# Kernel optimization log

Measured on AMD Instinct MI355X. Metric: run time of the kernel, lower is better.

## Reference

```python
import jax, jax.numpy as jnp
import numpy as np

K = 9  # neighbors per node (Dynamic_GraphConv2d k, dilation=1)


def setup_inputs() -> dict:
    key = jax.random.key(0)
    k1, k2 = jax.random.split(key, 2)
    x = jax.random.normal(k1, (2, 128, 64, 64), dtype=jnp.float32)
    # EdgeConv2d nn: 1x1 conv mapping 2*in_channels -> out_channels
    w = jax.random.normal(k2, (256, 256), dtype=jnp.float32) * 0.05  # [out, 2*in]
    b = jnp.zeros((256,), dtype=jnp.float32)
    return {"x": x, "w": w, "b": b}


def _knn_graph(xf, k):
    # xf: [B, C, N]. DenseDilatedKnnGraph L2-normalizes features before kNN.
    xn = xf * jax.lax.rsqrt(jnp.sum(xf * xf, axis=1, keepdims=True) + 1e-12)
    xt = jnp.transpose(xn, (0, 2, 1))                  # [B, N, C]
    sq = jnp.sum(xt * xt, axis=-1)                     # [B, N]
    inner = jnp.einsum('bnc,bmc->bnm', xt, xt)         # [B, N, N]
    neg_dist = 2.0 * inner - sq[:, :, None] - sq[:, None, :]
    _, nn_idx = jax.lax.top_k(neg_dist, k)             # [B, N, k] nearest neighbors
    return nn_idx


def reference(x, w, b):
    B, C, H, W = x.shape
    N = H * W
    xf = x.reshape(B, C, N)                            # nodes = flattened spatial dims
    nn_idx = _knn_graph(xf, K)
    # gather neighbor features x_j: [B, C, N, k]
    xt = jnp.transpose(xf, (0, 2, 1))                  # [B, N, C]
    x_j = jax.vmap(lambda t, i: t[i])(xt, nn_idx)      # [B, N, k, C]
    x_j = jnp.transpose(x_j, (0, 3, 1, 2))             # [B, C, N, k]
    x_i = xf[:, :, :, None]                            # center features [B, C, N, 1]
    # EdgeConv: max_k relu(W @ concat(x_i, x_j - x_i) + b)
    feat = jnp.concatenate(
        [jnp.broadcast_to(x_i, x_j.shape), x_j - x_i], axis=1)  # [B, 2C, N, k]
    out = jnp.einsum('oc,bcnk->bonk', w, feat) + b[None, :, None, None]
    out = jax.nn.relu(out)
    out = jnp.max(out, axis=-1)                        # [B, O, N]
    return out.reshape(B, -1, H, W)
```

## Files before the change

### kernel.cpp

```cpp
#include <hip/hip_runtime.h>
#include <float.h>

constexpr int CB = 2;
constexpr int CC = 128;
constexpr int CN = 4096;
constexpr int NSPLIT = 16;

typedef unsigned long long u64;
typedef unsigned int u32;

constexpr size_t OFF_SQ = 0;
constexpr size_t OFF_WT = OFF_SQ + (size_t)CB * CN;
constexpr size_t OFF_A  = OFF_WT + (size_t)CC * 512;
constexpr size_t OFF_PK = OFF_A + (size_t)CB * CN * 256;
constexpr size_t OFF_NN = OFF_PK + (size_t)CB * CN * NSPLIT * 12 / 1;

typedef __attribute__((ext_vector_type(8))) short bf16x8;
typedef __attribute__((ext_vector_type(4))) float f32x4;

__device__ __forceinline__ unsigned short f2bf(float f) {
    u32 u = __float_as_uint(f);
    u32 r = (u + 0x7FFFu + ((u >> 16) & 1u)) >> 16;
    return (unsigned short)r;
}
__device__ __forceinline__ float bf2f(unsigned short h) {
    return __uint_as_float(((u32)h) << 16);
}

__device__ __forceinline__ u32 mono32(float v) {
    u32 u = __float_as_uint(v);
    u32 m = (u32)((int)u >> 31);
    return u ^ (m | 0x80000000u);
}
__device__ __forceinline__ u64 make_key(float v, int jg) {
    return ((u64)mono32(v) << 12) | (u32)(4095 - jg);
}
__device__ __forceinline__ void key_insert(u64 (&sk)[9], u64 key) {
    u64 t = key;
#pragma unroll
    for (int k = 0; k < 9; ++k) {
        const bool gt = t > sk[k];
        const u64 hi = gt ? t : sk[k];
        t = gt ? sk[k] : t;
        sk[k] = hi;
    }
}
__device__ __forceinline__ void key_init(u64 (&sk)[9]) {
#pragma unroll
    for (int k = 0; k < 9; ++k) sk[k] = (u64)(8 - k);
}

__global__ __launch_bounds__(256) void prep_kernel(const float* __restrict__ x,
                                                   float* __restrict__ sqv,
                                                   unsigned short* __restrict__ xh,
                                                   unsigned short* __restrict__ xm,
                                                   unsigned short* __restrict__ xl) {
    __shared__ float XT[128][65];
    __shared__ float red[4][64];
    __shared__ float invl[64];
    const int b = blockIdx.y, n0 = blockIdx.x * 64;
    const int tid = threadIdx.x;
    const int nl = tid & 63, c0 = tid >> 6;
#pragma unroll 4
    for (int cc = 0; cc < 32; ++cc) {
        int c = cc * 4 + c0;
        XT[c][nl] = x[((size_t)(b * 128 + c)) * 4096 + n0 + nl];
    }
    __syncthreads();
    {
        float acc = 0.f;
#pragma unroll 4
        for (int cc = 0; cc < 32; ++cc) { float v = XT[c0 * 32 + cc][nl]; acc += v * v; }
        red[c0][nl] = acc;
    }
    __syncthreads();
    if (tid < 64) {
        float ss = red[0][tid] + red[1][tid] + red[2][tid] + red[3][tid] + 1e-12f;
        invl[tid] = 1.0f / sqrtf(ss);
    }
    __syncthreads();
    {
        float acc = 0.f;
        float iv = invl[nl];
#pragma unroll 4
        for (int cc = 0; cc < 32; ++cc) {
            int c = cc * 4 + c0;
            float v = XT[c][nl] * iv;
            XT[c][nl] = v;
            acc += v * v;
        }
        red[c0][nl] = acc;
    }
    __syncthreads();
    if (tid < 64) {
        sqv[b * 4096 + n0 + tid] = red[0][tid] + red[1][tid] + red[2][tid] + red[3][tid];
    }
    __syncthreads();
    {
        const int n = tid & 63, cq = tid >> 6;
        unsigned short hs[32], ms[32], ls[32];
#pragma unroll
        for (int cc = 0; cc < 32; ++cc) {
            float v = XT[cq * 32 + cc][n];
            unsigned short h = f2bf(v);  float hf = bf2f(h);
            float r1 = v - hf;
            unsigned short m = f2bf(r1); float mf = bf2f(m);
            unsigned short l = f2bf(r1 - mf);
            hs[cc] = h; ms[cc] = m; ls[cc] = l;
        }
        const int g = (n0 >> 4) + (n >> 4), r = n & 15;
        const size_t gb = ((size_t)(b * 256 + g)) * 2048 + r * 8;
#pragma unroll
        for (int u = 0; u < 4; ++u) {
            const size_t off = gb + (size_t)(cq * 4 + u) * 128;
            *(float4*)&xh[off] = *(const float4*)&hs[u * 8];
            *(float4*)&xm[off] = *(const float4*)&ms[u * 8];
            *(float4*)&xl[off] = *(const float4*)&ls[u * 8];
        }
    }
}

__global__ __launch_bounds__(256) void wprep_kernel(const float* __restrict__ w,
                                                    float* __restrict__ wt) {
    int id = blockIdx.x * 256 + threadIdx.x;
    int c = id >> 9, o = id & 511;
    float v;
    if (o < 256) v = w[o * 256 + c] - w[o * 256 + 128 + c];
    else         v = w[(o - 256) * 256 + 128 + c];
    wt[c * 512 + o] = v;
}

__global__ __launch_bounds__(256, 4) void knn_kernel(const unsigned short* __restrict__ xh,
                                                     const unsigned short* __restrict__ xm,
                                                     const unsigned short* __restrict__ xl,
                                                     const float* __restrict__ sqv,
                                                     u32* __restrict__ pk) {
    __shared__ u64 MK[2304];

    const int b  = blockIdx.z;
    const int i0 = blockIdx.y * 64;
    const int js = blockIdx.x;
    const int tid = threadIdx.x;
    const int lane = tid & 63, w = tid >> 6;
    const int l15 = lane & 15, l4 = lane >> 4;

    const size_t ib0 = ((size_t)(b * 256 + (i0 >> 4) + w)) * 2048;
    u64 sk[9];
    key_init(sk);

    for (int tt = 0; tt < 4; ++tt) {
        const int t = (tt + w) & 3;
        const int jt = js * 256 + t * 64;
        const size_t jb0 = ((size_t)(b * 256 + (jt >> 4))) * 2048;
        f32x4 a0 = {0.f, 0.f, 0.f, 0.f}, a1 = a0, a2 = a0, a3 = a0;

#pragma unroll
        for (int ch = 0; ch < 4; ++ch) {
            const int koff = (ch * 4 + l4) * 128 + l15 * 8;
            const bf16x8 ih = *(const bf16x8*)(xh + ib0 + koff);
            const bf16x8 im = *(const bf16x8*)(xm + ib0 + koff);
            const bf16x8 il = *(const bf16x8*)(xl + ib0 + koff);
#define DO_Y(ACC, Y)                                                          \
            {                                                                 \
                const bf16x8 jh = *(const bf16x8*)(xh + jb0 + (Y) * 2048 + koff); \
                const bf16x8 jm = *(const bf16x8*)(xm + jb0 + (Y) * 2048 + koff); \
                const bf16x8 jl = *(const bf16x8*)(xl + jb0 + (Y) * 2048 + koff); \
                ACC = __builtin_amdgcn_mfma_f32_16x16x32_bf16(jh, ih, ACC, 0, 0, 0); \
                ACC = __builtin_amdgcn_mfma_f32_16x16x32_bf16(jh, im, ACC, 0, 0, 0); \
                ACC = __builtin_amdgcn_mfma_f32_16x16x32_bf16(jm, ih, ACC, 0, 0, 0); \
                ACC = __builtin_amdgcn_mfma_f32_16x16x32_bf16(jm, im, ACC, 0, 0, 0); \
                ACC = __builtin_amdgcn_mfma_f32_16x16x32_bf16(jh, il, ACC, 0, 0, 0); \
                ACC = __builtin_amdgcn_mfma_f32_16x16x32_bf16(jl, ih, ACC, 0, 0, 0); \
            }
            DO_Y(a0, 0) DO_Y(a1, 1) DO_Y(a2, 2) DO_Y(a3, 3)
#undef DO_Y
        }
#define SCAN_Y(ACC, Y)                                                        \
        {                                                                     \
            const int jb4 = jt + (Y) * 16 + l4 * 4;                           \
            const float4 sq4 = *(const float4*)&sqv[b * 4096 + jb4];          \
            key_insert(sk, make_key(fmaf(2.0f, ACC[0], -sq4.x), jb4 + 0));    \
            key_insert(sk, make_key(fmaf(2.0f, ACC[1], -sq4.y), jb4 + 1));    \
            key_insert(sk, make_key(fmaf(2.0f, ACC[2], -sq4.z), jb4 + 2));    \
            key_insert(sk, make_key(fmaf(2.0f, ACC[3], -sq4.w), jb4 + 3));    \
        }
        SCAN_Y(a0, 0) SCAN_Y(a1, 1) SCAN_Y(a2, 2) SCAN_Y(a3, 3)
#undef SCAN_Y
    }
#pragma unroll
    for (int k = 0; k < 9; ++k) MK[tid * 9 + k] = sk[k];
    __syncthreads();
    if (tid < 64) {
        u64 mk[9];
        key_init(mk);
        const int wsrc = tid >> 4, r = tid & 15;
        for (int q2 = 0; q2 < 4; ++q2) {
            const int src = wsrc * 64 + q2 * 16 + r;
            for (int k = 0; k < 9; ++k) key_insert(mk, MK[src * 9 + k]);
        }
        u32 ow[12];
        u32 iw0 = 0, iw1 = 0, iw2 = 0;
#pragma unroll
        for (int k = 0; k < 9; ++k) {
            ow[k] = (u32)(mk[k] >> 12);
            u32 lj = (u32)((4095 - (int)(mk[k] & 4095)) - js * 256) & 255u;
            if (k < 4)      iw0 |= lj << (k * 8);
            else if (k < 8) iw1 |= lj << ((k - 4) * 8);
            else            iw2 |= lj;
        }
        ow[9] = iw0; ow[10] = iw1; ow[11] = iw2;
        const size_t base = ((size_t)(b * 4096 + i0 + tid) * NSPLIT + js) * 12;
        *(uint4*)&pk[base]     = *(const uint4*)&ow[0];
        *(uint4*)&pk[base + 4] = *(const uint4*)&ow[4];
        *(uint4*)&pk[base + 8] = *(const uint4*)&ow[8];
    }
}

__global__ __launch_bounds__(64) void merge_kernel(const u32* __restrict__ pk,
                                                   int* __restrict__ nn) {
    int t = blockIdx.x * 64 + threadIdx.x;
    u64 mk[9];
    key_init(mk);
    for (int s = 0; s < NSPLIT; ++s) {
        const u32* p = pk + ((size_t)t * NSPLIT + s) * 12;
        u32 ow[12];
        *(uint4*)&ow[0] = *(const uint4*)&p[0];
        *(uint4*)&ow[4] = *(const uint4*)&p[4];
        *(uint4*)&ow[8] = *(const uint4*)&p[8];
        const u32 iw[3] = {ow[9], ow[10], ow[11]};
#pragma unroll
        for (int k = 0; k < 9; ++k) {
            const int lj = (int)((iw[k >> 2] >> ((k & 3) * 8)) & 255u);
            const int jg = s * 256 + lj;
            const u64 key = ((u64)ow[k] << 12) | (u32)(4095 - jg);
            key_insert(mk, key);
        }
    }
#pragma unroll
    for (int k = 0; k < 9; ++k) nn[t * 9 + k] = 4095 - (int)(mk[k] & 4095);
}

__global__ __launch_bounds__(256, 2) void pq_kernel(const float* __restrict__ x,
                                                    const float* __restrict__ wt,
                                                    float* __restrict__ q,
                                                    float* __restrict__ out) {
    __shared__ float Xs[128][64];
    __shared__ float Ws[128][64];
    const int b = blockIdx.z;
    const int n0 = blockIdx.x * 64;
    const int o0 = blockIdx.y * 64;
    const int tid = threadIdx.x;
    {
        const int c4 = tid >> 4, j4 = (tid & 15) * 4;
#pragma unroll
        for (int cc = 0; cc < 8; ++cc) {
            int c = cc * 16 + c4;
            *(float4*)&Xs[c][j4] = *(const float4*)&x[((size_t)(b * 128 + c)) * 4096 + n0 + j4];
            *(float4*)&Ws[c][j4] = *(const float4*)&wt[c * 512 + o0 + j4];
        }
    }
    __syncthreads();
    const int tx = tid & 15, ty = tid >> 4;
    float acc[4][4];
#pragma unroll
    for (int i = 0; i < 4; ++i)
#pragma unroll
        for (int j = 0; j < 4; ++j) acc[i][j] = 0.f;
#pragma unroll 4
    for (int c = 0; c < 128; ++c) {
        const float4 av = *(const float4*)&Xs[c][ty * 4];
        const float4 bv = *(const float4*)&Ws[c][tx * 4];
        const float ar[4] = {av.x, av.y, av.z, av.w};
        const float br[4] = {bv.x, bv.y, bv.z, bv.w};
#pragma unroll
        for (int i = 0; i < 4; ++i)
#pragma unroll
            for (int j = 0; j < 4; ++j) acc[i][j] = fmaf(ar[i], br[j], acc[i][j]);
    }
    if (o0 < 256) {
#pragma unroll
        for (int j = 0; j < 4; ++j) {
            float4 v = make_float4(acc[0][j], acc[1][j], acc[2][j], acc[3][j]);
            *(float4*)&out[((size_t)(b * 256 + o0 + tx * 4 + j)) * 4096 + n0 + ty * 4] = v;
        }
    } else {
#pragma unroll
        for (int i = 0; i < 4; ++i) {
            float4 v = make_float4(acc[i][0], acc[i][1], acc[i][2], acc[i][3]);
            *(float4*)&q[((size_t)(b * 4096 + n0 + ty * 4 + i)) * 256 + (o0 - 256) + tx * 4] = v;
        }
    }
}

__global__ __launch_bounds__(256) void gather_kernel(const float* __restrict__ q,
                                                     const int* __restrict__ nn,
                                                     const float* __restrict__ bias,
                                                     float* __restrict__ out) {
    __shared__ int idx[32][9];
    const int b = blockIdx.y, n0 = blockIdx.x * 32;
    const int tid = threadIdx.x;
    for (int t = tid; t < 288; t += 256) {
        int pt = t / 9, k = t - pt * 9;
        idx[pt][k] = nn[(b * 4096 + n0 + pt) * 9 + k];
    }
    __syncthreads();
    const float bv = bias[tid];
    const size_t orow = ((size_t)(b * 256 + tid)) * 4096 + n0;
    float pvals[32];
#pragma unroll
    for (int u = 0; u < 8; ++u)
        *(float4*)&pvals[u * 4] = *(const float4*)&out[orow + u * 4];
    float val[32];
#pragma unroll
    for (int pt = 0; pt < 32; ++pt) {
        float m = -FLT_MAX;
#pragma unroll
        for (int k = 0; k < 9; ++k) {
            int j = idx[pt][k] & 4095;
            m = fmaxf(m, q[((size_t)(b * 4096 + j)) * 256 + tid]);
        }
        float vv = pvals[pt] + bv + m;
        val[pt] = vv > 0.f ? vv : 0.f;
    }
#pragma unroll
    for (int u = 0; u < 8; ++u) {
        float4 v = make_float4(val[u * 4], val[u * 4 + 1], val[u * 4 + 2], val[u * 4 + 3]);
        *(float4*)&out[orow + u * 4] = v;
    }
}

extern "C" void kernel_launch(void* const* d_in, const int* in_sizes, int n_in,
                              void* d_out, int out_size, void* d_ws, size_t ws_size,
                              hipStream_t stream) {
    const float* x    = (const float*)d_in[0];
    const float* w    = (const float*)d_in[1];
    const float* bias = (const float*)d_in[2];
    float* ws = (float*)d_ws;
    float* sq = ws + OFF_SQ;
    float* wt = ws + OFF_WT;
    unsigned short* xh = (unsigned short*)(ws + OFF_A);
    unsigned short* xm = xh + (size_t)CB * CN * CC;
    unsigned short* xl = xm + (size_t)CB * CN * CC;
    float* q  = ws + OFF_A;
    u32*   pk = (u32*)(ws + OFF_PK);
    int*   nn = (int*)(ws + OFF_NN);
    float* out = (float*)d_out;

    prep_kernel  <<<dim3(64, 2),     256, 0, stream>>>(x, sq, xh, xm, xl);
    wprep_kernel <<<dim3(256),       256, 0, stream>>>(w, wt);
    knn_kernel   <<<dim3(16, 64, 2), 256, 0, stream>>>(xh, xm, xl, sq, pk);
    merge_kernel <<<dim3(128),       64,  0, stream>>>(pk, nn);
    pq_kernel    <<<dim3(64, 8, 2),  256, 0, stream>>>(x, wt, q, out);
    gather_kernel<<<dim3(128, 2),    256, 0, stream>>>(q, nn, bias, out);
}
```

Measured before the change: 181.5 us.

## Move projection GEMM to split-bf16 MFMA and parallelize kNN merge

The fp32 shared-memory GEMM in pq_kernel is replaced by a 6-term split-bf16 (hi/mid/lo) MFMA product. It reuses the normalized x splits from the kNN prep and rescales by the stored row norm to undo the normalization. The weight prep now also emits bf16 hi/mid/lo in the MFMA fragment layout. The merge kernel uses two threads per row with a shuffle-based final merge, and knn_kernel occupancy hint rises to 8. The workspace is relaid so q no longer aliases the bf16 x buffers. The split-bf16 product may differ slightly in precision from fp32.

```diff
diff --git a/kernel.cpp b/kernel.cpp
--- a/kernel.cpp
+++ b/kernel.cpp
@@ -10,10 +10,11 @@
 typedef unsigned int u32;
 
 constexpr size_t OFF_SQ = 0;
-constexpr size_t OFF_WT = OFF_SQ + (size_t)CB * CN;
-constexpr size_t OFF_A  = OFF_WT + (size_t)CC * 512;
-constexpr size_t OFF_PK = OFF_A + (size_t)CB * CN * 256;
-constexpr size_t OFF_NN = OFF_PK + (size_t)CB * CN * NSPLIT * 12 / 1;
+constexpr size_t OFF_RN = 8192;
+constexpr size_t OFF_WP = 16384;
+constexpr size_t OFF_A  = 114688;
+constexpr size_t OFF_PK = OFF_A + 1572864;
+constexpr size_t OFF_NN = OFF_PK + 2097152;
 
 typedef __attribute__((ext_vector_type(8))) short bf16x8;
 typedef __attribute__((ext_vector_type(4))) float f32x4;
@@ -52,6 +53,7 @@
 
 __global__ __launch_bounds__(256) void prep_kernel(const float* __restrict__ x,
                                                    float* __restrict__ sqv,
+                                                   float* __restrict__ rnv,
                                                    unsigned short* __restrict__ xh,
                                                    unsigned short* __restrict__ xm,
                                                    unsigned short* __restrict__ xl) {
@@ -76,7 +78,9 @@
     __syncthreads();
     if (tid < 64) {
         float ss = red[0][tid] + red[1][tid] + red[2][tid] + red[3][tid] + 1e-12f;
-        invl[tid] = 1.0f / sqrtf(ss);
+        float sr = sqrtf(ss);
+        invl[tid] = 1.0f / sr;
+        rnv[b * 4096 + n0 + tid] = sr;
     }
     __syncthreads();
     {
@@ -121,16 +125,23 @@
 }
 
 __global__ __launch_bounds__(256) void wprep_kernel(const float* __restrict__ w,
-                                                    float* __restrict__ wt) {
+                                                    unsigned short* __restrict__ wh,
+                                                    unsigned short* __restrict__ wm,
+                                                    unsigned short* __restrict__ wl) {
     int id = blockIdx.x * 256 + threadIdx.x;
     int c = id >> 9, o = id & 511;
     float v;
     if (o < 256) v = w[o * 256 + c] - w[o * 256 + 128 + c];
     else         v = w[(o - 256) * 256 + 128 + c];
-    wt[c * 512 + o] = v;
-}
-
-__global__ __launch_bounds__(256, 4) void knn_kernel(const unsigned short* __restrict__ xh,
+    unsigned short h = f2bf(v);  float hf = bf2f(h);
+    float r1 = v - hf;
+    unsigned short m = f2bf(r1); float mf = bf2f(m);
+    unsigned short l = f2bf(r1 - mf);
+    const size_t off = (size_t)(o >> 4) * 2048 + (c >> 3) * 128 + (o & 15) * 8 + (c & 7);
+    wh[off] = h; wm[off] = m; wl[off] = l;
+}
+
+__global__ __launch_bounds__(256, 8) void knn_kernel(const unsigned short* __restrict__ xh,
                                                      const unsigned short* __restrict__ xm,
                                                      const unsigned short* __restrict__ xl,
                                                      const float* __restrict__ sqv,
@@ -216,13 +227,14 @@
     }
 }
 
-__global__ __launch_bounds__(64) void merge_kernel(const u32* __restrict__ pk,
-                                                   int* __restrict__ nn) {
-    int t = blockIdx.x * 64 + threadIdx.x;
+__global__ __launch_bounds__(256) void merge_kernel(const u32* __restrict__ pk,
+                                                    int* __restrict__ nn) {
+    const int gt = blockIdx.x * 256 + threadIdx.x;
+    const int row = gt >> 1, half = gt & 1;
     u64 mk[9];
     key_init(mk);
-    for (int s = 0; s < NSPLIT; ++s) {
-        const u32* p = pk + ((size_t)t * NSPLIT + s) * 12;
+    for (int s = half * 8; s < half * 8 + 8; ++s) {
+        const u32* p = pk + ((size_t)row * NSPLIT + s) * 12;
         u32 ow[12];
         *(uint4*)&ow[0] = *(const uint4*)&p[0];
         *(uint4*)&ow[4] = *(const uint4*)&p[4];
@@ -232,64 +244,89 @@
         for (int k = 0; k < 9; ++k) {
             const int lj = (int)((iw[k >> 2] >> ((k & 3) * 8)) & 255u);
             const int jg = s * 256 + lj;
-            const u64 key = ((u64)ow[k] << 12) | (u32)(4095 - jg);
-            key_insert(mk, key);
-        }
-    }
-#pragma unroll
-    for (int k = 0; k < 9; ++k) nn[t * 9 + k] = 4095 - (int)(mk[k] & 4095);
-}
-
-__global__ __launch_bounds__(256, 2) void pq_kernel(const float* __restrict__ x,
-                                                    const float* __restrict__ wt,
+            key_insert(mk, ((u64)ow[k] << 12) | (u32)(4095 - jg));
+        }
+    }
+    u64 tmp[9];
+#pragma unroll
+    for (int k = 0; k < 9; ++k) tmp[k] = __shfl_xor(mk[k], 1);
+#pragma unroll
+    for (int k = 0; k < 9; ++k) key_insert(mk, tmp[k]);
+    if (half == 0) {
+#pragma unroll
+        for (int k = 0; k < 9; ++k) nn[row * 9 + k] = 4095 - (int)(mk[k] & 4095);
+    }
+}
+
+__global__ __launch_bounds__(256, 4) void pq_kernel(const unsigned short* __restrict__ xh,
+                                                    const unsigned short* __restrict__ xm,
+                                                    const unsigned short* __restrict__ xl,
+                                                    const unsigned short* __restrict__ wh,
+                                                    const unsigned short* __restrict__ wm,
+                                                    const unsigned short* __restrict__ wl,
+                                                    const float* __restrict__ rnv,
                                                     float* __restrict__ q,
                                                     float* __restrict__ out) {
-    __shared__ float Xs[128][64];
-    __shared__ float Ws[128][64];
-    const int b = blockIdx.z;
+    const int b  = blockIdx.z;
     const int n0 = blockIdx.x * 64;
     const int o0 = blockIdx.y * 64;
     const int tid = threadIdx.x;
-    {
-        const int c4 = tid >> 4, j4 = (tid & 15) * 4;
-#pragma unroll
-        for (int cc = 0; cc < 8; ++cc) {
-            int c = cc * 16 + c4;
-            *(float4*)&Xs[c][j4] = *(const float4*)&x[((size_t)(b * 128 + c)) * 4096 + n0 + j4];
-            *(float4*)&Ws[c][j4] = *(const float4*)&wt[c * 512 + o0 + j4];
-        }
-    }
-    __syncthreads();
-    const int tx = tid & 15, ty = tid >> 4;
-    float acc[4][4];
-#pragma unroll
-    for (int i = 0; i < 4; ++i)
-#pragma unroll
-        for (int j = 0; j < 4; ++j) acc[i][j] = 0.f;
-#pragma unroll 4
-    for (int c = 0; c < 128; ++c) {
-        const float4 av = *(const float4*)&Xs[c][ty * 4];
-        const float4 bv = *(const float4*)&Ws[c][tx * 4];
-        const float ar[4] = {av.x, av.y, av.z, av.w};
-        const float br[4] = {bv.x, bv.y, bv.z, bv.w};
-#pragma unroll
-        for (int i = 0; i < 4; ++i)
-#pragma unroll
-            for (int j = 0; j < 4; ++j) acc[i][j] = fmaf(ar[i], br[j], acc[i][j]);
-    }
-    if (o0 < 256) {
-#pragma unroll
-        for (int j = 0; j < 4; ++j) {
-            float4 v = make_float4(acc[0][j], acc[1][j], acc[2][j], acc[3][j]);
-            *(float4*)&out[((size_t)(b * 256 + o0 + tx * 4 + j)) * 4096 + n0 + ty * 4] = v;
-        }
-    } else {
-#pragma unroll
-        for (int i = 0; i < 4; ++i) {
-            float4 v = make_float4(acc[i][0], acc[i][1], acc[i][2], acc[i][3]);
-            *(float4*)&q[((size_t)(b * 4096 + n0 + ty * 4 + i)) * 256 + (o0 - 256) + tx * 4] = v;
-        }
-    }
+    const int lane = tid & 63, w = tid >> 6;
+    const int l15 = lane & 15, l4 = lane >> 4;
+    const int nw = n0 + (w & 1) * 32;
+    const int ow = o0 + (w >> 1) * 32;
+
+    const size_t xg = ((size_t)(b * 256 + (nw >> 4))) * 2048;
+    const size_t wg = ((size_t)(ow >> 4)) * 2048;
+
+    f32x4 a00 = {0.f, 0.f, 0.f, 0.f}, a01 = a00, a10 = a00, a11 = a00;
+
+#pragma unroll
+    for (int ch = 0; ch < 4; ++ch) {
+        const int koff = (ch * 4 + l4) * 128 + l15 * 8;
+        const bf16x8 x0h = *(const bf16x8*)(xh + xg + koff);
+        const bf16x8 x0m = *(const bf16x8*)(xm + xg + koff);
+        const bf16x8 x0l = *(const bf16x8*)(xl + xg + koff);
+        const bf16x8 x1h = *(const bf16x8*)(xh + xg + 2048 + koff);
+        const bf16x8 x1m = *(const bf16x8*)(xm + xg + 2048 + koff);
+        const bf16x8 x1l = *(const bf16x8*)(xl + xg + 2048 + koff);
+        const bf16x8 w0h = *(const bf16x8*)(wh + wg + koff);
+        const bf16x8 w0m = *(const bf16x8*)(wm + wg + koff);
+        const bf16x8 w0l = *(const bf16x8*)(wl + wg + koff);
+        const bf16x8 w1h = *(const bf16x8*)(wh + wg + 2048 + koff);
+        const bf16x8 w1m = *(const bf16x8*)(wm + wg + 2048 + koff);
+        const bf16x8 w1l = *(const bf16x8*)(wl + wg + 2048 + koff);
+#define PROD(ACC, WH, WM, WL, XH, XM, XL)                                     \
+        ACC = __builtin_amdgcn_mfma_f32_16x16x32_bf16(WH, XH, ACC, 0, 0, 0);  \
+        ACC = __builtin_amdgcn_mfma_f32_16x16x32_bf16(WH, XM, ACC, 0, 0, 0);  \
+        ACC = __builtin_amdgcn_mfma_f32_16x16x32_bf16(WM, XH, ACC, 0, 0, 0);  \
+        ACC = __builtin_amdgcn_mfma_f32_16x16x32_bf16(WM, XM, ACC, 0, 0, 0);  \
+        ACC = __builtin_amdgcn_mfma_f32_16x16x32_bf16(WH, XL, ACC, 0, 0, 0);  \
+        ACC = __builtin_amdgcn_mfma_f32_16x16x32_bf16(WL, XH, ACC, 0, 0, 0);
+        PROD(a00, w0h, w0m, w0l, x0h, x0m, x0l)
+        PROD(a01, w0h, w0m, w0l, x1h, x1m, x1l)
+        PROD(a10, w1h, w1m, w1l, x0h, x0m, x0l)
+        PROD(a11, w1h, w1m, w1l, x1h, x1m, x1l)
+#undef PROD
+    }
+#define EPI(ACC, TO, TN)                                                      \
+    {                                                                         \
+        const int ob = ow + (TO) * 16 + l4 * 4;                               \
+        const int n  = nw + (TN) * 16 + l15;                                  \
+        const float rn = rnv[b * 4096 + n];                                   \
+        if (ob < 256) {                                                       \
+            out[((size_t)(b * 256 + ob + 0)) * 4096 + n] = ACC[0] * rn;       \
+            out[((size_t)(b * 256 + ob + 1)) * 4096 + n] = ACC[1] * rn;       \
+            out[((size_t)(b * 256 + ob + 2)) * 4096 + n] = ACC[2] * rn;       \
+            out[((size_t)(b * 256 + ob + 3)) * 4096 + n] = ACC[3] * rn;       \
+        } else {                                                              \
+            float4 v = make_float4(ACC[0] * rn, ACC[1] * rn,                  \
+                                   ACC[2] * rn, ACC[3] * rn);                 \
+            *(float4*)&q[((size_t)(b * 4096 + n)) * 256 + (ob - 256)] = v;    \
+        }                                                                     \
+    }
+    EPI(a00, 0, 0) EPI(a01, 0, 1) EPI(a10, 1, 0) EPI(a11, 1, 1)
+#undef EPI
 }
 
 __global__ __launch_bounds__(256) void gather_kernel(const float* __restrict__ q,
@@ -337,19 +374,22 @@
     const float* bias = (const float*)d_in[2];
     float* ws = (float*)d_ws;
     float* sq = ws + OFF_SQ;
-    float* wt = ws + OFF_WT;
+    float* rn = ws + OFF_RN;
+    unsigned short* wh = (unsigned short*)(ws + OFF_WP);
+    unsigned short* wm = wh + 65536;
+    unsigned short* wl = wm + 65536;
     unsigned short* xh = (unsigned short*)(ws + OFF_A);
     unsigned short* xm = xh + (size_t)CB * CN * CC;
     unsigned short* xl = xm + (size_t)CB * CN * CC;
-    float* q  = ws + OFF_A;
     u32*   pk = (u32*)(ws + OFF_PK);
+    float* q  = ws + OFF_PK;
     int*   nn = (int*)(ws + OFF_NN);
     float* out = (float*)d_out;
 
-    prep_kernel  <<<dim3(64, 2),     256, 0, stream>>>(x, sq, xh, xm, xl);
-    wprep_kernel <<<dim3(256),       256, 0, stream>>>(w, wt);
+    prep_kernel  <<<dim3(64, 2),     256, 0, stream>>>(x, sq, rn, xh, xm, xl);
+    wprep_kernel <<<dim3(256),       256, 0, stream>>>(w, wh, wm, wl);
     knn_kernel   <<<dim3(16, 64, 2), 256, 0, stream>>>(xh, xm, xl, sq, pk);
-    merge_kernel <<<dim3(128),       64,  0, stream>>>(pk, nn);
-    pq_kernel    <<<dim3(64, 8, 2),  256, 0, stream>>>(x, wt, q, out);
+    merge_kernel <<<dim3(64),        256, 0, stream>>>(pk, nn);
+    pq_kernel    <<<dim3(64, 8, 2),  256, 0, stream>>>(xh, xm, xl, wh, wm, wl, rn, q, out);
     gather_kernel<<<dim3(128, 2),    256, 0, stream>>>(q, nn, bias, out);
 }
```

After: 310.3 us. 1.71x slower.
